# Kernel tuning notes

Measured on AMD Instinct MI355X. Metric: run time of the kernel, lower is better.

## Reference

```python
import jax, jax.numpy as jnp
import numpy as np

B, T, D, K, CAND = 1024, 256, 128, 4, 500
NEG = float(-2**32 + 1)
EPS = 1e-3  # keras LayerNormalization default epsilon

def ln(x, g, b):
    mu = jnp.mean(x, axis=-1, keepdims=True)
    var = jnp.mean(jnp.square(x - mu), axis=-1, keepdims=True)
    return (x - mu) * jax.lax.rsqrt(var + EPS) * g + b

def setup_inputs() -> dict:
    key = jax.random.key(0)
    ks = jax.random.split(key, 12)
    s = 0.05
    inp = {
        'item_his_eb': jax.random.normal(ks[0], (B, T, D), jnp.float32),
        'mask': jax.random.randint(ks[1], (B, T), 0, 2, jnp.int32),
        'W1': jax.random.normal(ks[2], (D, D), jnp.float32) * s,
        'W2': jax.random.normal(ks[3], (D,), jnp.float32) * s,
        'W3': jax.random.normal(ks[4], (D, D), jnp.float32) * s,
        'W4': jax.random.normal(ks[5], (D,), jnp.float32) * s,
        'W_k1': jax.random.normal(ks[6], (K, D, D), jnp.float32) * s,
        'W_k2': jax.random.normal(ks[7], (K, D), jnp.float32) * s,
        'C': jax.random.normal(ks[8], (CAND, D), jnp.float32) * s,
        'pos_emb': jax.random.normal(ks[9], (1, T, D), jnp.float32) * s,
        'g1': jnp.ones((D,), jnp.float32), 'b1': jnp.zeros((D,), jnp.float32),
        'g2': jnp.ones((D,), jnp.float32), 'b2': jnp.zeros((D,), jnp.float32),
        'g3': jnp.ones((D,), jnp.float32), 'b3': jnp.zeros((D,), jnp.float32),
        'g4': jnp.ones((D,), jnp.float32), 'b4': jnp.zeros((D,), jnp.float32),
    }
    return inp

def reference(item_his_eb, mask, W1, W2, W3, W4, W_k1, W_k2, C, pos_emb,
              g1, b1, g2, b2, g3, b3, g4, b4):
    num_interest = W_k1.shape[0]
    m0 = (mask == 0)  # [B,T] padding positions
    x = item_his_eb + pos_emb  # [B,T,D]

    # Concept activation
    hidden = jnp.tanh(jnp.einsum('bte,ea->bta', x, W1))
    att = jnp.einsum('bte,e->bt', hidden, W2)
    a = jax.nn.softmax(jnp.where(m0, NEG, att), axis=-1)
    z_u = jnp.einsum('bte,bt->be', x, a)
    s_u = jnp.einsum('be,ce->bc', z_u, C)  # [B,CAND]
    s_u_k, idx = jax.lax.top_k(s_u, num_interest)  # sorted descending
    c_u = C[idx] * jax.nn.sigmoid(s_u_k)[..., None]  # [B,K,D]

    # Interest embedding generation
    h1 = jnp.einsum('bte,ea->bta', x, W3)
    h1 = jnp.einsum('bte,bke->btk', ln(h1, g1, b1), ln(c_u, g2, b2))
    h1 = jnp.where(m0[:, :, None], NEG, h1)
    P_kt = jnp.transpose(jax.nn.softmax(h1, axis=-1), (0, 2, 1))  # [B,K,T]
    h2 = jnp.tanh(jnp.einsum('bte,kea->bkta', x, W_k1))
    h2 = jnp.einsum('bkte,ke->bkt', h2, W_k2)
    h2 = jnp.where(m0[:, None, :], NEG, h2)
    P_tk = jax.nn.softmax(h2, axis=-1)  # softmax over t
    P = P_kt * P_tk
    interest_emb = ln(jnp.einsum('bte,bkt->bke', x, P), g3, b3)  # [B,K,D]

    # Interest aggregation
    P_u = jnp.transpose(P_kt, (0, 2, 1))  # [B,T,K]
    X_hat = jnp.einsum('btk,bke->bte', P_u, c_u)
    h3 = jnp.tanh(jnp.einsum('bte,ea->bta', X_hat, W3))
    h3 = jnp.einsum('bte,e->bt', h3, W4)
    h3 = jax.nn.softmax(jnp.where(m0, NEG, h3), axis=-1)
    c_apt = ln(jnp.einsum('bte,bt->be', X_hat, h3), g4, b4)
    e_u = jax.nn.softmax(jnp.einsum('be,bke->bk', c_apt, interest_emb) / 0.1, axis=-1)
    v_u = jnp.einsum('bke,bk->be', interest_emb, e_u)
    return v_u
```

## Files before the change

kernel.cpp:

```cpp
#include <hip/hip_runtime.h>
#include <hip/hip_bf16.h>
#include <string.h>

#define BB 1024
#define TT 256
#define DD 128
#define KK 4
#define CC 500
#define NEGF (-4294967296.0f)
#define EPSL 1e-3f

typedef __attribute__((ext_vector_type(8))) short bf16x8;
typedef __attribute__((ext_vector_type(4))) float f32x4;


__device__ __forceinline__ float fast_tanh(float x){
  float ax = fabsf(x);
  float e  = __expf(2.0f * ax);
  float t  = 1.0f - 2.0f * __builtin_amdgcn_rcpf(e + 1.0f);
  return copysignf(t, x);
}

__device__ __forceinline__ unsigned short bfbits(float f){
  __hip_bfloat16 h = __float2bfloat16(f);
  unsigned short u;
  memcpy(&u, &h, 2);
  return u;
}
__device__ __forceinline__ float bf2f(unsigned short u){
  return __uint_as_float(((unsigned)u) << 16);
}

__device__ __forceinline__ float wave_sum(float v){
  #pragma unroll
  for (int o = 32; o > 0; o >>= 1) v += __shfl_xor(v, o);
  return v;
}
__device__ __forceinline__ float wave_max(float v){
  #pragma unroll
  for (int o = 32; o > 0; o >>= 1) v = fmaxf(v, __shfl_xor(v, o));
  return v;
}


__global__ __launch_bounds__(256) void k_wpack(
    const float* __restrict__ W1, const float* __restrict__ W3,
    const float* __restrict__ Wk1,
    uint4* __restrict__ whi, uint4* __restrict__ wlo)
{
  int gid = blockIdx.x * 256 + threadIdx.x;
  int lane = gid & 63;
  int frag = gid >> 6;
  int n = frag & 7, kt = (frag >> 3) & 3, w = frag >> 5;
  const float* Wp = (w == 0) ? W1 : (w == 1) ? W3 : (Wk1 + (long)(w - 2) * DD * DD);
  int col = n * 16 + (lane & 15);
  int k0 = kt * 32 + (lane >> 4) * 8;
  unsigned int H[4], L[4];
  #pragma unroll
  for (int d = 0; d < 4; ++d){
    float v0 = Wp[(long)(k0 + 2 * d) * DD + col];
    float v1 = Wp[(long)(k0 + 2 * d + 1) * DD + col];
    unsigned short h0 = bfbits(v0); unsigned short l0 = bfbits(v0 - bf2f(h0));
    unsigned short h1 = bfbits(v1); unsigned short l1 = bfbits(v1 - bf2f(h1));
    H[d] = (unsigned)h0 | ((unsigned)h1 << 16);
    L[d] = (unsigned)l0 | ((unsigned)l1 << 16);
  }
  whi[gid] = make_uint4(H[0], H[1], H[2], H[3]);
  wlo[gid] = make_uint4(L[0], L[1], L[2], L[3]);
}


__global__ __launch_bounds__(256) void k_prep(
    const float* __restrict__ W3, const float* __restrict__ Cmat,
    float* __restrict__ W3T, float* __restrict__ CT)
{
  int gid = blockIdx.x * 256 + threadIdx.x;
  if (gid < DD * DD){
    int a = gid >> 7, e = gid & 127;
    W3T[gid] = W3[e * DD + a];
  } else {
    int j = gid - DD * DD;
    if (j < DD * CC){
      int e = j / CC, c = j - e * CC;
      CT[j] = Cmat[c * DD + e];
    }
  }
}


__global__ __launch_bounds__(512, 4) void k_big6m(
    const float* __restrict__ item, const float* __restrict__ pos,
    const uint4* __restrict__ whi, const uint4* __restrict__ wlo,
    const float* __restrict__ W2, const float* __restrict__ Wk2,
    float* __restrict__ att, float* __restrict__ h2log, float* __restrict__ lnstats)
{
  __shared__ uint4 smem4[4096];
  __shared__ float dscr[5][128][2];
  __shared__ float sscr[2][128][2];
  char* smem = (char*)smem4;
  const int tid = threadIdx.x, lane = tid & 63, wv = tid >> 6;
  const int ni = wv & 1, mi = wv >> 1;
  const long rbase = (long)blockIdx.x * 128;
  const int r15 = lane & 15, g = lane >> 4;
  const f32x4 ZV = {0.f, 0.f, 0.f, 0.f};

  #pragma unroll
  for (int it = 0; it < 4; ++it){
    int cid = tid + it * 512;
    int row = cid >> 4, c0 = (cid & 15) * 8;
    const float* src = item + (rbase + row) * DD + c0;
    const float* ps  = pos + (int)((rbase + row) & 255) * DD + c0;
    float4 f0 = *(const float4*)src;
    float4 f1 = *(const float4*)(src + 4);
    float4 p0 = *(const float4*)ps;
    float4 p1 = *(const float4*)(ps + 4);
    float v[8] = {f0.x + p0.x, f0.y + p0.y, f0.z + p0.z, f0.w + p0.w,
                  f1.x + p1.x, f1.y + p1.y, f1.z + p1.z, f1.w + p1.w};
    unsigned int H[4], L[4];
    #pragma unroll
    for (int d = 0; d < 4; ++d){
      unsigned short h0 = bfbits(v[2 * d]);     unsigned short l0 = bfbits(v[2 * d]     - bf2f(h0));
      unsigned short h1 = bfbits(v[2 * d + 1]); unsigned short l1 = bfbits(v[2 * d + 1] - bf2f(h1));
      H[d] = (unsigned)h0 | ((unsigned)h1 << 16);
      L[d] = (unsigned)l0 | ((unsigned)l1 << 16);
    }
    int byt = (c0 * 2) ^ ((row & 7) << 4);
    *(uint4*)(smem + row * 256 + byt)         = make_uint4(H[0], H[1], H[2], H[3]);
    *(uint4*)(smem + 32768 + row * 256 + byt) = make_uint4(L[0], L[1], L[2], L[3]);
  }
  __syncthreads();

  const int wrow = mi * 32;
  const int WL6[6] = {0, 2, 3, 4, 5, 1};

  uint4 PBh[2][4], PBl[2][4];
  {
    const uint4* bhp = whi + (long)(ni * 4) * 64 + lane;
    const uint4* blp = wlo + (long)(ni * 4) * 64 + lane;
    #pragma unroll
    for (int n = 0; n < 4; ++n){ PBh[0][n] = bhp[n * 64]; PBl[0][n] = blp[n * 64]; }
  }

  #pragma unroll
  for (int wi = 0; wi < 6; ++wi){
    const int w = WL6[wi];
    f32x4 acc[2][4];
    #pragma unroll
    for (int m = 0; m < 2; ++m)
      #pragma unroll
      for (int n = 0; n < 4; ++n) acc[m][n] = ZV;

    #pragma unroll
    for (int kt = 0; kt < 4; ++kt){
      const int gidx = wi * 4 + kt;
      const int cur = gidx & 1, nxt = cur ^ 1;

      if (gidx < 23){
        const int gn = gidx + 1;
        const int wn = WL6[gn >> 2], ktn = gn & 3;
        const uint4* bhp = whi + (long)((wn * 4 + ktn) * 8 + ni * 4) * 64 + lane;
        const uint4* blp = wlo + (long)((wn * 4 + ktn) * 8 + ni * 4) * 64 + lane;
        #pragma unroll
        for (int n = 0; n < 4; ++n){ PBh[nxt][n] = bhp[n * 64]; PBl[nxt][n] = blp[n * 64]; }
      }

      bf16x8 ah[2], al[2];
      #pragma unroll
      for (int m = 0; m < 2; ++m){
        int row = wrow + m * 16 + r15;
        int byt = (kt * 64 + g * 16) ^ ((row & 7) << 4);
        ah[m] = *(const bf16x8*)(smem + row * 256 + byt);
        al[m] = *(const bf16x8*)(smem + 32768 + row * 256 + byt);
      }
      #pragma unroll
      for (int n = 0; n < 4; ++n){
        bf16x8 bh = *(const bf16x8*)&PBh[cur][n];
        bf16x8 bl = *(const bf16x8*)&PBl[cur][n];
        #pragma unroll
        for (int m = 0; m < 2; ++m){
          acc[m][n] = __builtin_amdgcn_mfma_f32_16x16x32_bf16(ah[m], bh, acc[m][n], 0, 0, 0);
          acc[m][n] = __builtin_amdgcn_mfma_f32_16x16x32_bf16(ah[m], bl, acc[m][n], 0, 0, 0);
          acc[m][n] = __builtin_amdgcn_mfma_f32_16x16x32_bf16(al[m], bh, acc[m][n], 0, 0, 0);
        }
      }
    }

    if (w != 1){
      const float* vp = (w == 0) ? W2 : (Wk2 + (w - 2) * DD);
      float pd[2][4] = {{0, 0, 0, 0}, {0, 0, 0, 0}};
      #pragma unroll
      for (int n = 0; n < 4; ++n){
        float vv = vp[ni * 64 + n * 16 + r15];
        #pragma unroll
        for (int m = 0; m < 2; ++m)
          #pragma unroll
          for (int j = 0; j < 4; ++j)
            pd[m][j] = fmaf(fast_tanh(acc[m][n][j]), vv, pd[m][j]);
      }
      #pragma unroll
      for (int m = 0; m < 2; ++m)
        #pragma unroll
        for (int j = 0; j < 4; ++j){
          float v = pd[m][j];
          v += __shfl_xor(v, 1); v += __shfl_xor(v, 2);
          v += __shfl_xor(v, 4); v += __shfl_xor(v, 8);
          if (r15 == 0) dscr[wi][wrow + m * 16 + g * 4 + j][ni] = v;
        }
    } else {
      #pragma unroll
      for (int m = 0; m < 2; ++m)
        #pragma unroll
        for (int j = 0; j < 4; ++j){
          float s = 0.f, q = 0.f;
          #pragma unroll
          for (int n = 0; n < 4; ++n){
            float y = acc[m][n][j];
            s += y; q = fmaf(y, y, q);
          }
          s += __shfl_xor(s, 1); s += __shfl_xor(s, 2);
          s += __shfl_xor(s, 4); s += __shfl_xor(s, 8);
          q += __shfl_xor(q, 1); q += __shfl_xor(q, 2);
          q += __shfl_xor(q, 4); q += __shfl_xor(q, 8);
          if (r15 == 0){
            int row = wrow + m * 16 + g * 4 + j;
            sscr[0][row][ni] = s;
            sscr[1][row][ni] = q;
          }
        }
    }
  }
  __syncthreads();

  if (tid < 128){
    long rg = rbase + tid;
    long b = rg >> 8; int t = (int)(rg & 255);
    att[rg] = dscr[0][tid][0] + dscr[0][tid][1];
    #pragma unroll
    for (int wi = 1; wi < 5; ++wi)
      h2log[(b * KK + (wi - 1)) * TT + t] = dscr[wi][tid][0] + dscr[wi][tid][1];
    float s = sscr[0][tid][0] + sscr[0][tid][1];
    float q = sscr[1][tid][0] + sscr[1][tid][1];
    float mu = s * (1.f / DD);
    float var = q * (1.f / DD) - mu * mu;
    float rs = rsqrtf(var + EPSL);
    float2 st; st.x = mu; st.y = rs;
    *(float2*)&lnstats[rg * 2] = st;
  }
}


__global__ __launch_bounds__(256, 4) void k_fused(
    const float* __restrict__ item, const float* __restrict__ pos,
    const int* __restrict__ mask, const float* __restrict__ att,
    const float* __restrict__ h2log, const float* __restrict__ lnstats,
    const float* __restrict__ Cmat, const float* __restrict__ CT,
    const float* __restrict__ W3, const float* __restrict__ W3T,
    const float* __restrict__ g1, const float* __restrict__ b1,
    const float* __restrict__ g2, const float* __restrict__ b2,
    const float* __restrict__ g3, const float* __restrict__ b3,
    const float* __restrict__ g4, const float* __restrict__ b4,
    const float* __restrict__ W4, float* __restrict__ out)
{
  __shared__ float arena[4096];
  __shared__ float pkt_s[KK][TT];
  __shared__ float P_s[KK][TT];
  __shared__ float lnc_s[KK][DD];
  __shared__ float cu_s[KK][DD];
  __shared__ float vk_s[KK][DD];
  __shared__ float cw3s[KK][DD];
  __shared__ float ies_s[KK][DD];
  __shared__ float a_s[TT];
  __shared__ int   m0s[TT];
  __shared__ float g1s[DD], b1s[DD];
  __shared__ float cas[DD], w4s[DD];
  __shared__ float rbuf[32];
  __shared__ float sel_v[KK];
  __shared__ int   sel_i[KK];
  __shared__ float SkTk[2][KK];

  const int tid = threadIdx.x;
  const long b = blockIdx.x;
  const int lane = tid & 63, wv = tid >> 6;

  float attv = att[b * TT + tid];
  int   mk   = mask[b * TT + tid];
  if (tid < DD){ g1s[tid] = g1[tid]; b1s[tid] = b1[tid]; }
  m0s[tid] = (mk == 0);

  {
    float v = (mk == 0) ? NEGF : attv;
    float wm = wave_max(v);
    if (lane == 0) rbuf[wv] = wm;
    __syncthreads();
    float mx = fmaxf(fmaxf(rbuf[0], rbuf[1]), fmaxf(rbuf[2], rbuf[3]));
    float ex = __expf(v - mx);
    float ws = wave_sum(ex);
    if (lane == 0) rbuf[4 + wv] = ws;
    __syncthreads();
    float sm = rbuf[4] + rbuf[5] + rbuf[6] + rbuf[7];
    a_s[tid] = ex / sm;
  }
  __syncthreads();

  const float4* item4 = (const float4*)(item + (long)b * TT * DD);
  const float4* pos4  = (const float4*)pos;

  {
    int q = tid & 31, h = tid >> 5;
    float4 acc = {0.f, 0.f, 0.f, 0.f};
    for (int t = h; t < TT; t += 8){
      float4 xi = item4[t * 32 + q];
      float4 pp = pos4[t * 32 + q];
      float av = a_s[t];
      acc.x = fmaf(av, xi.x + pp.x, acc.x);
      acc.y = fmaf(av, xi.y + pp.y, acc.y);
      acc.z = fmaf(av, xi.z + pp.z, acc.z);
      acc.w = fmaf(av, xi.w + pp.w, acc.w);
    }
    *(float4*)&arena[h * 128 + q * 4] = acc;
    __syncthreads();
    if (tid < DD){
      float z = 0.f;
      #pragma unroll
      for (int h2 = 0; h2 < 8; ++h2) z += arena[h2 * 128 + tid];
      arena[1024 + tid] = z;
    }
    __syncthreads();
  }
  float* zs  = arena + 1024;
  float* s_s = arena + 1152;

  for (int c = tid; c < 512; c += 256){
    float s = -3.0e38f;
    if (c < CC){
      s = 0.f;
      for (int e = 0; e < DD; ++e) s = fmaf(zs[e], CT[e * CC + c], s);
    }
    s_s[c] = s;
  }
  __syncthreads();

  for (int k = 0; k < KK; ++k){
    float bv = -3.0e38f; int bi = 1 << 20;
    for (int c = tid; c < 512; c += 256){
      float sv = s_s[c];
      if (sv > bv || (sv == bv && c < bi)){ bv = sv; bi = c; }
    }
    #pragma unroll
    for (int o = 32; o > 0; o >>= 1){
      float ov = __shfl_xor(bv, o); int oi = __shfl_xor(bi, o);
      if (ov > bv || (ov == bv && oi < bi)){ bv = ov; bi = oi; }
    }
    if (lane == 0){ rbuf[wv] = bv; ((int*)rbuf)[8 + wv] = bi; }
    __syncthreads();
    if (tid == 0){
      float xv = rbuf[0]; int xi = ((int*)rbuf)[8];
      #pragma unroll
      for (int w2 = 1; w2 < 4; ++w2){
        float ov = rbuf[w2]; int oi = ((int*)rbuf)[8 + w2];
        if (ov > xv || (ov == xv && oi < xi)){ xv = ov; xi = oi; }
      }
      sel_v[k] = xv; sel_i[k] = xi; s_s[xi] = -3.0e38f;
    }
    __syncthreads();
  }

  {
    int k = wv, e0 = lane, e1 = lane + 64;
    float sig = 1.f / (1.f + __expf(-sel_v[k]));
    long ci = (long)sel_i[k] * DD;
    float c0 = Cmat[ci + e0] * sig, c1 = Cmat[ci + e1] * sig;
    cu_s[k][e0] = c0; cu_s[k][e1] = c1;
    float mean = wave_sum(c0 + c1) * (1.f / DD);
    float d0 = c0 - mean, d1 = c1 - mean;
    float var = wave_sum(d0 * d0 + d1 * d1) * (1.f / DD);
    float rs = rsqrtf(var + EPSL);
    float l0 = d0 * rs * g2[e0] + b2[e0];
    float l1 = d1 * rs * g2[e1] + b2[e1];
    lnc_s[k][e0] = l0; lnc_s[k][e1] = l1;
    float gl0 = g1s[e0] * l0, gl1 = g1s[e1] * l1;
    float S = wave_sum(gl0 + gl1);
    float T = wave_sum(b1s[e0] * l0 + b1s[e1] * l1);
    if (lane == 0){ SkTk[0][k] = S; SkTk[1][k] = T; }
    cw3s[k][e0] = gl0; cw3s[k][e1] = gl1;
    float v0 = 0.f, v1 = 0.f;
    for (int a = 0; a < DD; ++a){
      float gv = cw3s[k][a];
      v0 = fmaf(W3T[a * DD + e0], gv, v0);
      v1 = fmaf(W3T[a * DD + e1], gv, v1);
    }
    vk_s[k][e0] = v0; vk_s[k][e1] = v1;
  }
  __syncthreads();

  for (int step = 0; step < 16; ++step){
    int t = step * 16 + wv * 4 + (lane >> 4);
    int e0 = (lane & 15) * 8;
    const float* xr = item + ((long)b * TT + t) * DD + e0;
    const float* pr = pos + t * DD + e0;
    float4 xa = *(const float4*)xr, xb = *(const float4*)(xr + 4);
    float4 pa = *(const float4*)pr, pb = *(const float4*)(pr + 4);
    float x0 = xa.x + pa.x, x1 = xa.y + pa.y, x2 = xa.z + pa.z, x3 = xa.w + pa.w;
    float x4 = xb.x + pb.x, x5 = xb.y + pb.y, x6 = xb.z + pb.z, x7 = xb.w + pb.w;
    float2 st = *(const float2*)&lnstats[((long)b * TT + t) * 2];
    float h[KK];
    #pragma unroll
    for (int k = 0; k < KK; ++k){
      float4 v0 = *(const float4*)&vk_s[k][e0];
      float4 v1 = *(const float4*)&vk_s[k][e0 + 4];
      float pk = x0 * v0.x + x1 * v0.y + x2 * v0.z + x3 * v0.w
               + x4 * v1.x + x5 * v1.y + x6 * v1.z + x7 * v1.w;
      pk += __shfl_xor(pk, 1); pk += __shfl_xor(pk, 2);
      pk += __shfl_xor(pk, 4); pk += __shfl_xor(pk, 8);
      h[k] = st.y * (pk - st.x * SkTk[0][k]) + SkTk[1][k];
    }
    float p[KK];
    if (m0s[t]){
      p[0] = p[1] = p[2] = p[3] = 0.25f;
    } else {
      float mxh = fmaxf(fmaxf(h[0], h[1]), fmaxf(h[2], h[3]));
      float sme = 0.f;
      #pragma unroll
      for (int k = 0; k < KK; ++k){ p[k] = __expf(h[k] - mxh); sme += p[k]; }
      float inv = 1.f / sme;
      #pragma unroll
      for (int k = 0; k < KK; ++k) p[k] *= inv;
    }
    int kk = lane & 15;
    if (kk < KK) pkt_s[kk][t] = p[kk];
  }
  __syncthreads();

  {
    int k = wv;
    float4 vj = *(const float4*)&h2log[((long)b * KK + k) * TT + lane * 4];
    float v0 = m0s[lane * 4 + 0] ? NEGF : vj.x;
    float v1 = m0s[lane * 4 + 1] ? NEGF : vj.y;
    float v2 = m0s[lane * 4 + 2] ? NEGF : vj.z;
    float v3 = m0s[lane * 4 + 3] ? NEGF : vj.w;
    float mxv = wave_max(fmaxf(fmaxf(v0, v1), fmaxf(v2, v3)));
    float e0 = __expf(v0 - mxv), e1 = __expf(v1 - mxv);
    float e2 = __expf(v2 - mxv), e3 = __expf(v3 - mxv);
    float sm = wave_sum(e0 + e1 + e2 + e3);
    float inv = 1.f / sm;
    float4 pk4 = *(const float4*)&pkt_s[k][lane * 4];
    float4 r;
    r.x = pk4.x * e0 * inv; r.y = pk4.y * e1 * inv;
    r.z = pk4.z * e2 * inv; r.w = pk4.w * e3 * inv;
    *(float4*)&P_s[k][lane * 4] = r;
  }
  __syncthreads();

  {
    int q = tid & 31, h = tid >> 5;
    float4 ak[KK];
    #pragma unroll
    for (int k = 0; k < KK; ++k) ak[k] = {0.f, 0.f, 0.f, 0.f};
    for (int t = h; t < TT; t += 8){
      float4 xi = item4[t * 32 + q];
      float4 pp = pos4[t * 32 + q];
      float4 xv; xv.x = xi.x + pp.x; xv.y = xi.y + pp.y; xv.z = xi.z + pp.z; xv.w = xi.w + pp.w;
      #pragma unroll
      for (int k = 0; k < KK; ++k){
        float pv = P_s[k][t];
        ak[k].x = fmaf(pv, xv.x, ak[k].x); ak[k].y = fmaf(pv, xv.y, ak[k].y);
        ak[k].z = fmaf(pv, xv.z, ak[k].z); ak[k].w = fmaf(pv, xv.w, ak[k].w);
      }
    }
    #pragma unroll
    for (int k = 0; k < KK; ++k)
      *(float4*)&arena[h * 512 + k * 128 + q * 4] = ak[k];
    __syncthreads();
    int e = tid & 127, kh = tid >> 7;
    for (int k2 = kh; k2 < KK; k2 += 2){
      float s = 0.f;
      #pragma unroll
      for (int h2 = 0; h2 < 8; ++h2) s += arena[h2 * 512 + k2 * 128 + e];
      ies_s[k2][e] = s;
    }
  }
  __syncthreads();

  {
    int k = wv, e0 = lane, e1 = lane + 64;
    float v0 = ies_s[k][e0], v1 = ies_s[k][e1];
    float mean = wave_sum(v0 + v1) * (1.f / DD);
    float d0 = v0 - mean, d1 = v1 - mean;
    float var = wave_sum(d0 * d0 + d1 * d1) * (1.f / DD);
    float rs = rsqrtf(var + EPSL);
    ies_s[k][e0] = d0 * rs * g3[e0] + b3[e0];
    ies_s[k][e1] = d1 * rs * g3[e1] + b3[e1];
    float s0 = 0.f, s1 = 0.f;
    for (int e = 0; e < DD; ++e){
      float cv = cu_s[k][e];
      s0 = fmaf(cv, W3[e * DD + e0], s0);
      s1 = fmaf(cv, W3[e * DD + e1], s1);
    }
    cw3s[k][e0] = s0; cw3s[k][e1] = s1;
  }
  if (tid < DD) w4s[tid] = W4[tid];
  __syncthreads();

  float pk0 = pkt_s[0][tid], pk1 = pkt_s[1][tid], pk2 = pkt_s[2][tid], pk3 = pkt_s[3][tid];
  float sv = 0.f;
  for (int a = 0; a < DD; ++a){
    float hp = pk0 * cw3s[0][a] + pk1 * cw3s[1][a] + pk2 * cw3s[2][a] + pk3 * cw3s[3][a];
    sv = fmaf(fast_tanh(hp), w4s[a], sv);
  }
  float h3;
  {
    float v = m0s[tid] ? NEGF : sv;
    float wm = wave_max(v);
    if (lane == 0) rbuf[wv] = wm;
    __syncthreads();
    float mx = fmaxf(fmaxf(rbuf[0], rbuf[1]), fmaxf(rbuf[2], rbuf[3]));
    float ex = __expf(v - mx);
    float ws = wave_sum(ex);
    if (lane == 0) rbuf[4 + wv] = ws;
    __syncthreads();
    float sm = rbuf[4] + rbuf[5] + rbuf[6] + rbuf[7];
    h3 = ex / sm;
  }
  __syncthreads();
  {
    float w0 = wave_sum(pk0 * h3), w1 = wave_sum(pk1 * h3);
    float w2 = wave_sum(pk2 * h3), w3 = wave_sum(pk3 * h3);
    if (lane == 0){
      rbuf[8 + wv * 4 + 0] = w0; rbuf[8 + wv * 4 + 1] = w1;
      rbuf[8 + wv * 4 + 2] = w2; rbuf[8 + wv * 4 + 3] = w3;
    }
  }
  __syncthreads();
  float wk0 = rbuf[8] + rbuf[12] + rbuf[16] + rbuf[20];
  float wk1 = rbuf[9] + rbuf[13] + rbuf[17] + rbuf[21];
  float wk2 = rbuf[10] + rbuf[14] + rbuf[18] + rbuf[22];
  float wk3 = rbuf[11] + rbuf[15] + rbuf[19] + rbuf[23];
  {
    float cp = 0.f;
    if (tid < DD)
      cp = wk0 * cu_s[0][tid] + wk1 * cu_s[1][tid] + wk2 * cu_s[2][tid] + wk3 * cu_s[3][tid];
    float ws = wave_sum((tid < DD) ? cp : 0.f);
    if (lane == 0) rbuf[wv] = ws;
    __syncthreads();
    float mean = (rbuf[0] + rbuf[1] + rbuf[2] + rbuf[3]) * (1.f / DD);
    float d = (tid < DD) ? cp - mean : 0.f;
    float wq = wave_sum(d * d);
    if (lane == 0) rbuf[4 + wv] = wq;
    __syncthreads();
    float var = (rbuf[4] + rbuf[5] + rbuf[6] + rbuf[7]) * (1.f / DD);
    float rs = rsqrtf(var + EPSL);
    if (tid < DD) cas[tid] = d * rs * g4[tid] + b4[tid];
  }
  __syncthreads();
  {
    float c0 = (tid < DD) ? cas[tid] * ies_s[0][tid] : 0.f;
    float c1 = (tid < DD) ? cas[tid] * ies_s[1][tid] : 0.f;
    float c2 = (tid < DD) ? cas[tid] * ies_s[2][tid] : 0.f;
    float c3 = (tid < DD) ? cas[tid] * ies_s[3][tid] : 0.f;
    float w0 = wave_sum(c0), w1 = wave_sum(c1), w2 = wave_sum(c2), w3 = wave_sum(c3);
    if (lane == 0){
      rbuf[8 + wv * 4 + 0] = w0; rbuf[8 + wv * 4 + 1] = w1;
      rbuf[8 + wv * 4 + 2] = w2; rbuf[8 + wv * 4 + 3] = w3;
    }
    __syncthreads();
    float l0 = (rbuf[8] + rbuf[12] + rbuf[16] + rbuf[20]) * 10.f;
    float l1 = (rbuf[9] + rbuf[13] + rbuf[17] + rbuf[21]) * 10.f;
    float l2 = (rbuf[10] + rbuf[14] + rbuf[18] + rbuf[22]) * 10.f;
    float l3 = (rbuf[11] + rbuf[15] + rbuf[19] + rbuf[23]) * 10.f;
    float mx2 = fmaxf(fmaxf(l0, l1), fmaxf(l2, l3));
    float e0 = __expf(l0 - mx2), e1 = __expf(l1 - mx2);
    float e2 = __expf(l2 - mx2), e3 = __expf(l3 - mx2);
    float inv = 1.f / (e0 + e1 + e2 + e3);
    if (tid < DD){
      float r = (ies_s[0][tid] * e0 + ies_s[1][tid] * e1 +
                 ies_s[2][tid] * e2 + ies_s[3][tid] * e3) * inv;
      out[b * DD + tid] = r;
    }
  }
}


extern "C" void kernel_launch(void* const* d_in, const int* in_sizes, int n_in,
                              void* d_out, int out_size, void* d_ws, size_t ws_size,
                              hipStream_t stream)
{
  const float* item = (const float*)d_in[0];
  const int*   mask = (const int*)d_in[1];
  const float* W1   = (const float*)d_in[2];
  const float* W2   = (const float*)d_in[3];
  const float* W3   = (const float*)d_in[4];
  const float* W4   = (const float*)d_in[5];
  const float* Wk1  = (const float*)d_in[6];
  const float* Wk2  = (const float*)d_in[7];
  const float* Cm   = (const float*)d_in[8];
  const float* pos  = (const float*)d_in[9];
  const float* g1   = (const float*)d_in[10]; const float* b1 = (const float*)d_in[11];
  const float* g2   = (const float*)d_in[12]; const float* b2 = (const float*)d_in[13];
  const float* g3   = (const float*)d_in[14]; const float* b3 = (const float*)d_in[15];
  const float* g4   = (const float*)d_in[16]; const float* b4 = (const float*)d_in[17];
  float* out = (float*)d_out;

  char* p = (char*)d_ws;
  float* att     = (float*)(p);
  float* h2log   = (float*)(p + 1048576);
  float* lnstats = (float*)(p + 5242880);
  float* W3T     = (float*)(p + 7340032);
  float* CT      = (float*)(p + 7405568);
  uint4* whi = (uint4*)d_out;
  uint4* wlo = whi + 12288;
  (void)in_sizes; (void)n_in; (void)out_size; (void)ws_size;

  k_wpack <<<dim3(48),  dim3(256), 0, stream>>>(W1, W3, Wk1, whi, wlo);
  k_prep  <<<dim3(314), dim3(256), 0, stream>>>(W3, Cm, W3T, CT);
  k_big6m <<<dim3((BB * TT) / 128), dim3(512), 0, stream>>>(item, pos, whi, wlo, W2, Wk2,
                                                            att, h2log, lnstats);
  k_fused <<<dim3(BB), dim3(256), 0, stream>>>(item, pos, mask, att, h2log, lnstats,
                                               Cm, CT, W3, W3T,
                                               g1, b1, g2, b2, g3, b3, g4, b4, W4, out);
}
```

Measured before the change: 288.7 us.

## Retile k_big6m warps to 2x4 layout and drop weight prefetch double-buffer

Result: slower. 299.1 us (+3.6%).

```diff
diff --git a/kernel.cpp b/kernel.cpp
--- a/kernel.cpp
+++ b/kernel.cpp
@@ -95,11 +95,11 @@
     float* __restrict__ att, float* __restrict__ h2log, float* __restrict__ lnstats)
 {
   __shared__ uint4 smem4[4096];
-  __shared__ float dscr[5][128][2];
-  __shared__ float sscr[2][128][2];
+  __shared__ float dscr[5][128][4];
+  __shared__ float sscr[2][128][4];
   char* smem = (char*)smem4;
   const int tid = threadIdx.x, lane = tid & 63, wv = tid >> 6;
-  const int ni = wv & 1, mi = wv >> 1;
+  const int ni = wv & 3, mi = wv >> 2;
   const long rbase = (long)blockIdx.x * 128;
   const int r15 = lane & 15, g = lane >> 4;
   const f32x4 ZV = {0.f, 0.f, 0.f, 0.f};
@@ -130,54 +130,37 @@
   }
   __syncthreads();
 
-  const int wrow = mi * 32;
+  const int wrow = mi * 64;
   const int WL6[6] = {0, 2, 3, 4, 5, 1};
-
-  uint4 PBh[2][4], PBl[2][4];
-  {
-    const uint4* bhp = whi + (long)(ni * 4) * 64 + lane;
-    const uint4* blp = wlo + (long)(ni * 4) * 64 + lane;
-    #pragma unroll
-    for (int n = 0; n < 4; ++n){ PBh[0][n] = bhp[n * 64]; PBl[0][n] = blp[n * 64]; }
-  }
 
   #pragma unroll
   for (int wi = 0; wi < 6; ++wi){
     const int w = WL6[wi];
-    f32x4 acc[2][4];
-    #pragma unroll
-    for (int m = 0; m < 2; ++m)
-      #pragma unroll
-      for (int n = 0; n < 4; ++n) acc[m][n] = ZV;
+    f32x4 acc[4][2];
+    #pragma unroll
+    for (int m = 0; m < 4; ++m)
+      #pragma unroll
+      for (int n = 0; n < 2; ++n) acc[m][n] = ZV;
 
     #pragma unroll
     for (int kt = 0; kt < 4; ++kt){
-      const int gidx = wi * 4 + kt;
-      const int cur = gidx & 1, nxt = cur ^ 1;
-
-      if (gidx < 23){
-        const int gn = gidx + 1;
-        const int wn = WL6[gn >> 2], ktn = gn & 3;
-        const uint4* bhp = whi + (long)((wn * 4 + ktn) * 8 + ni * 4) * 64 + lane;
-        const uint4* blp = wlo + (long)((wn * 4 + ktn) * 8 + ni * 4) * 64 + lane;
-        #pragma unroll
-        for (int n = 0; n < 4; ++n){ PBh[nxt][n] = bhp[n * 64]; PBl[nxt][n] = blp[n * 64]; }
-      }
-
-      bf16x8 ah[2], al[2];
-      #pragma unroll
-      for (int m = 0; m < 2; ++m){
+      bf16x8 ah[4], al[4];
+      #pragma unroll
+      for (int m = 0; m < 4; ++m){
         int row = wrow + m * 16 + r15;
         int byt = (kt * 64 + g * 16) ^ ((row & 7) << 4);
         ah[m] = *(const bf16x8*)(smem + row * 256 + byt);
         al[m] = *(const bf16x8*)(smem + 32768 + row * 256 + byt);
       }
-      #pragma unroll
-      for (int n = 0; n < 4; ++n){
-        bf16x8 bh = *(const bf16x8*)&PBh[cur][n];
-        bf16x8 bl = *(const bf16x8*)&PBl[cur][n];
+      const uint4* bhp = whi + (long)((w * 4 + kt) * 8 + ni * 2) * 64 + lane;
+      const uint4* blp = wlo + (long)((w * 4 + kt) * 8 + ni * 2) * 64 + lane;
+      #pragma unroll
+      for (int n = 0; n < 2; ++n){
+        uint4 bhu = bhp[n * 64], blu = blp[n * 64];
+        bf16x8 bh = *(const bf16x8*)&bhu;
+        bf16x8 bl = *(const bf16x8*)&blu;
         #pragma unroll
-        for (int m = 0; m < 2; ++m){
+        for (int m = 0; m < 4; ++m){
           acc[m][n] = __builtin_amdgcn_mfma_f32_16x16x32_bf16(ah[m], bh, acc[m][n], 0, 0, 0);
           acc[m][n] = __builtin_amdgcn_mfma_f32_16x16x32_bf16(ah[m], bl, acc[m][n], 0, 0, 0);
           acc[m][n] = __builtin_amdgcn_mfma_f32_16x16x32_bf16(al[m], bh, acc[m][n], 0, 0, 0);
@@ -187,18 +170,18 @@
 
     if (w != 1){
       const float* vp = (w == 0) ? W2 : (Wk2 + (w - 2) * DD);
-      float pd[2][4] = {{0, 0, 0, 0}, {0, 0, 0, 0}};
-      #pragma unroll
-      for (int n = 0; n < 4; ++n){
-        float vv = vp[ni * 64 + n * 16 + r15];
+      float pd[4][4] = {{0,0,0,0},{0,0,0,0},{0,0,0,0},{0,0,0,0}};
+      #pragma unroll
+      for (int n = 0; n < 2; ++n){
+        float vv = vp[ni * 32 + n * 16 + r15];
         #pragma unroll
-        for (int m = 0; m < 2; ++m)
+        for (int m = 0; m < 4; ++m)
           #pragma unroll
           for (int j = 0; j < 4; ++j)
             pd[m][j] = fmaf(fast_tanh(acc[m][n][j]), vv, pd[m][j]);
       }
       #pragma unroll
-      for (int m = 0; m < 2; ++m)
+      for (int m = 0; m < 4; ++m)
         #pragma unroll
         for (int j = 0; j < 4; ++j){
           float v = pd[m][j];
@@ -208,12 +191,12 @@
         }
     } else {
       #pragma unroll
-      for (int m = 0; m < 2; ++m)
+      for (int m = 0; m < 4; ++m)
         #pragma unroll
         for (int j = 0; j < 4; ++j){
           float s = 0.f, q = 0.f;
           #pragma unroll
-          for (int n = 0; n < 4; ++n){
+          for (int n = 0; n < 2; ++n){
             float y = acc[m][n][j];
             s += y; q = fmaf(y, y, q);
           }
@@ -234,12 +217,13 @@
   if (tid < 128){
     long rg = rbase + tid;
     long b = rg >> 8; int t = (int)(rg & 255);
-    att[rg] = dscr[0][tid][0] + dscr[0][tid][1];
+    att[rg] = (dscr[0][tid][0] + dscr[0][tid][1]) + (dscr[0][tid][2] + dscr[0][tid][3]);
     #pragma unroll
     for (int wi = 1; wi < 5; ++wi)
-      h2log[(b * KK + (wi - 1)) * TT + t] = dscr[wi][tid][0] + dscr[wi][tid][1];
-    float s = sscr[0][tid][0] + sscr[0][tid][1];
-    float q = sscr[1][tid][0] + sscr[1][tid][1];
+      h2log[(b * KK + (wi - 1)) * TT + t] =
+        (dscr[wi][tid][0] + dscr[wi][tid][1]) + (dscr[wi][tid][2] + dscr[wi][tid][3]);
+    float s = (sscr[0][tid][0] + sscr[0][tid][1]) + (sscr[0][tid][2] + sscr[0][tid][3]);
+    float q = (sscr[1][tid][0] + sscr[1][tid][1]) + (sscr[1][tid][2] + sscr[1][tid][3]);
     float mu = s * (1.f / DD);
     float var = q * (1.f / DD) - mu * mu;
     float rs = rsqrtf(var + EPSL);
```

## Merge prep kernels, drop B-fragment register prefetch, stagger weight order and set priority

Applied to the files above, without the earlier changes.

New measurement: 300.9 us. 4.2% more time.

```diff
diff --git a/kernel.cpp b/kernel.cpp
--- a/kernel.cpp
+++ b/kernel.cpp
@@ -43,46 +43,43 @@
 }
 
 
-__global__ __launch_bounds__(256) void k_wpack(
+__global__ __launch_bounds__(256) void k_preppack(
     const float* __restrict__ W1, const float* __restrict__ W3,
-    const float* __restrict__ Wk1,
-    uint4* __restrict__ whi, uint4* __restrict__ wlo)
-{
-  int gid = blockIdx.x * 256 + threadIdx.x;
-  int lane = gid & 63;
-  int frag = gid >> 6;
-  int n = frag & 7, kt = (frag >> 3) & 3, w = frag >> 5;
-  const float* Wp = (w == 0) ? W1 : (w == 1) ? W3 : (Wk1 + (long)(w - 2) * DD * DD);
-  int col = n * 16 + (lane & 15);
-  int k0 = kt * 32 + (lane >> 4) * 8;
-  unsigned int H[4], L[4];
-  #pragma unroll
-  for (int d = 0; d < 4; ++d){
-    float v0 = Wp[(long)(k0 + 2 * d) * DD + col];
-    float v1 = Wp[(long)(k0 + 2 * d + 1) * DD + col];
-    unsigned short h0 = bfbits(v0); unsigned short l0 = bfbits(v0 - bf2f(h0));
-    unsigned short h1 = bfbits(v1); unsigned short l1 = bfbits(v1 - bf2f(h1));
-    H[d] = (unsigned)h0 | ((unsigned)h1 << 16);
-    L[d] = (unsigned)l0 | ((unsigned)l1 << 16);
-  }
-  whi[gid] = make_uint4(H[0], H[1], H[2], H[3]);
-  wlo[gid] = make_uint4(L[0], L[1], L[2], L[3]);
-}
-
-
-__global__ __launch_bounds__(256) void k_prep(
-    const float* __restrict__ W3, const float* __restrict__ Cmat,
+    const float* __restrict__ Wk1, const float* __restrict__ Cmat,
+    uint4* __restrict__ whi, uint4* __restrict__ wlo,
     float* __restrict__ W3T, float* __restrict__ CT)
 {
   int gid = blockIdx.x * 256 + threadIdx.x;
-  if (gid < DD * DD){
-    int a = gid >> 7, e = gid & 127;
-    W3T[gid] = W3[e * DD + a];
+  if (gid < 12288){
+    int lane = gid & 63;
+    int frag = gid >> 6;
+    int n = frag & 7, kt = (frag >> 3) & 3, w = frag >> 5;
+    const float* Wp = (w == 0) ? W1 : (w == 1) ? W3 : (Wk1 + (long)(w - 2) * DD * DD);
+    int col = n * 16 + (lane & 15);
+    int k0 = kt * 32 + (lane >> 4) * 8;
+    unsigned int H[4], L[4];
+    #pragma unroll
+    for (int d = 0; d < 4; ++d){
+      float v0 = Wp[(long)(k0 + 2 * d) * DD + col];
+      float v1 = Wp[(long)(k0 + 2 * d + 1) * DD + col];
+      unsigned short h0 = bfbits(v0); unsigned short l0 = bfbits(v0 - bf2f(h0));
+      unsigned short h1 = bfbits(v1); unsigned short l1 = bfbits(v1 - bf2f(h1));
+      H[d] = (unsigned)h0 | ((unsigned)h1 << 16);
+      L[d] = (unsigned)l0 | ((unsigned)l1 << 16);
+    }
+    whi[gid] = make_uint4(H[0], H[1], H[2], H[3]);
+    wlo[gid] = make_uint4(L[0], L[1], L[2], L[3]);
   } else {
-    int j = gid - DD * DD;
-    if (j < DD * CC){
-      int e = j / CC, c = j - e * CC;
-      CT[j] = Cmat[c * DD + e];
+    int j = gid - 12288;
+    if (j < DD * DD){
+      int a = j >> 7, e = j & 127;
+      W3T[j] = W3[e * DD + a];
+    } else {
+      j -= DD * DD;
+      if (j < DD * CC){
+        int e = j / CC, c = j - e * CC;
+        CT[j] = Cmat[c * DD + e];
+      }
     }
   }
 }
@@ -132,17 +129,11 @@
 
   const int wrow = mi * 32;
   const int WL6[6] = {0, 2, 3, 4, 5, 1};
-
-  uint4 PBh[2][4], PBl[2][4];
-  {
-    const uint4* bhp = whi + (long)(ni * 4) * 64 + lane;
-    const uint4* blp = wlo + (long)(ni * 4) * 64 + lane;
-    #pragma unroll
-    for (int n = 0; n < 4; ++n){ PBh[0][n] = bhp[n * 64]; PBl[0][n] = blp[n * 64]; }
-  }
-
-  #pragma unroll
-  for (int wi = 0; wi < 6; ++wi){
+  const int roff = 3 * ni;
+
+  #pragma unroll 1
+  for (int wi0 = 0; wi0 < 6; ++wi0){
+    const int wi = (wi0 + roff) % 6;
     const int w = WL6[wi];
     f32x4 acc[2][4];
     #pragma unroll
@@ -150,20 +141,9 @@
       #pragma unroll
       for (int n = 0; n < 4; ++n) acc[m][n] = ZV;
 
+    __builtin_amdgcn_s_setprio(1);
     #pragma unroll
     for (int kt = 0; kt < 4; ++kt){
-      const int gidx = wi * 4 + kt;
-      const int cur = gidx & 1, nxt = cur ^ 1;
-
-      if (gidx < 23){
-        const int gn = gidx + 1;
-        const int wn = WL6[gn >> 2], ktn = gn & 3;
-        const uint4* bhp = whi + (long)((wn * 4 + ktn) * 8 + ni * 4) * 64 + lane;
-        const uint4* blp = wlo + (long)((wn * 4 + ktn) * 8 + ni * 4) * 64 + lane;
-        #pragma unroll
-        for (int n = 0; n < 4; ++n){ PBh[nxt][n] = bhp[n * 64]; PBl[nxt][n] = blp[n * 64]; }
-      }
-
       bf16x8 ah[2], al[2];
       #pragma unroll
       for (int m = 0; m < 2; ++m){
@@ -172,10 +152,13 @@
         ah[m] = *(const bf16x8*)(smem + row * 256 + byt);
         al[m] = *(const bf16x8*)(smem + 32768 + row * 256 + byt);
       }
+      const uint4* bhp = whi + (long)((w * 4 + kt) * 8 + ni * 4) * 64 + lane;
+      const uint4* blp = wlo + (long)((w * 4 + kt) * 8 + ni * 4) * 64 + lane;
       #pragma unroll
       for (int n = 0; n < 4; ++n){
-        bf16x8 bh = *(const bf16x8*)&PBh[cur][n];
-        bf16x8 bl = *(const bf16x8*)&PBl[cur][n];
+        uint4 bhu = bhp[n * 64], blu = blp[n * 64];
+        bf16x8 bh = *(const bf16x8*)&bhu;
+        bf16x8 bl = *(const bf16x8*)&blu;
         #pragma unroll
         for (int m = 0; m < 2; ++m){
           acc[m][n] = __builtin_amdgcn_mfma_f32_16x16x32_bf16(ah[m], bh, acc[m][n], 0, 0, 0);
@@ -184,6 +167,7 @@
         }
       }
     }
+    __builtin_amdgcn_s_setprio(0);
 
     if (w != 1){
       const float* vp = (w == 0) ? W2 : (Wk2 + (w - 2) * DD);
@@ -610,11 +594,10 @@
   uint4* wlo = whi + 12288;
   (void)in_sizes; (void)n_in; (void)out_size; (void)ws_size;
 
-  k_wpack <<<dim3(48),  dim3(256), 0, stream>>>(W1, W3, Wk1, whi, wlo);
-  k_prep  <<<dim3(314), dim3(256), 0, stream>>>(W3, Cm, W3T, CT);
-  k_big6m <<<dim3((BB * TT) / 128), dim3(512), 0, stream>>>(item, pos, whi, wlo, W2, Wk2,
-                                                            att, h2log, lnstats);
-  k_fused <<<dim3(BB), dim3(256), 0, stream>>>(item, pos, mask, att, h2log, lnstats,
-                                               Cm, CT, W3, W3T,
-                                               g1, b1, g2, b2, g3, b3, g4, b4, W4, out);
-}
+  k_preppack <<<dim3(362), dim3(256), 0, stream>>>(W1, W3, Wk1, Cm, whi, wlo, W3T, CT);
+  k_big6m    <<<dim3((BB * TT) / 128), dim3(512), 0, stream>>>(item, pos, whi, wlo, W2, Wk2,
+                                                               att, h2log, lnstats);
+  k_fused    <<<dim3(BB), dim3(256), 0, stream>>>(item, pos, mask, att, h2log, lnstats,
+                                                  Cm, CT, W3, W3T,
+                                                  g1, b1, g2, b2, g3, b3, g4, b4, W4, out);
+}
```
